# Performance work log

Measured on AMD Instinct MI355X. Metric: run time of the kernel, lower is better.

## Reference

```python
import jax, jax.numpy as jnp
import numpy as np


def _conv1x1(x, w):
    # bias-free 1x1 conv == channel-mixing GEMM: w:(out,in), x:(b,in,h,w)
    return jnp.einsum('oc,bchw->bohw', w, x)


def setup_inputs() -> dict:
    key = jax.random.key(0)
    k = jax.random.split(key, 5)
    C, IC = 512, 256  # channel, inter_channel = channel // 2
    x = jax.random.normal(k[0], (8, C, 64, 64), dtype=jnp.float32)
    s = 0.02
    return {
        'x': x,
        'w_phi': jax.random.normal(k[1], (IC, C), dtype=jnp.float32) * s,
        'w_theta': jax.random.normal(k[2], (IC, C), dtype=jnp.float32) * s,
        'w_g': jax.random.normal(k[3], (IC, C), dtype=jnp.float32) * s,
        'w_mask': jax.random.normal(k[4], (C, IC), dtype=jnp.float32) * s,
    }


def reference(x, w_phi, w_theta, w_g, w_mask):
    b, c, h, wd = x.shape
    hw = h * wd
    ic = c // 2
    # Faithful to the torch source: conv outputs have c//2 channels but are
    # viewed as (b, c, -1) -> (b, c, hw//2); tokens axis is hw//2, feat dim c.
    n = hw // 2
    phi = _conv1x1(x, w_phi).reshape(b, c, n)                      # (b, c, n)
    theta = _conv1x1(x, w_theta).reshape(b, c, n).transpose(0, 2, 1)  # (b, n, c)
    g = _conv1x1(x, w_g).reshape(b, c, n).transpose(0, 2, 1)          # (b, n, c)
    attn = jnp.einsum('bnc,bcm->bnm', theta, phi)                  # (b, n, n)
    attn = jax.nn.softmax(attn, axis=1)                            # torch Softmax(dim=1)
    out = jnp.einsum('bnm,bmc->bnc', attn, g)                      # (b, n, c)
    out = out.transpose(0, 2, 1).reshape(b, ic, h, wd)             # (b, c//2, h, w)
    return _conv1x1(out, w_mask) + x
```

## Files before the change

### kernel.cpp

```cpp
#include <hip/hip_runtime.h>

typedef unsigned short u16;
typedef __bf16 bf16x8 __attribute__((ext_vector_type(8)));
typedef unsigned short u16x8 __attribute__((ext_vector_type(8)));
typedef float f32x4 __attribute__((ext_vector_type(4)));

__device__ __forceinline__ u16 f2bf(float f) {
    unsigned u = __float_as_uint(f);
    unsigned r = u + 0x7fffu + ((u >> 16) & 1u);
    return (u16)(r >> 16);
}
__device__ __forceinline__ float bf2f(u16 v) {
    return __uint_as_float(((unsigned)v) << 16);
}

__device__ __forceinline__ void async16(const void* g, void* l) {
    __builtin_amdgcn_global_load_lds(
        (__attribute__((address_space(1))) void*)(unsigned long long)g,
        (__attribute__((address_space(3))) void*)l, 16, 0, 0);
}

__device__ __forceinline__ bf16x8 ld8(const u16* p) {
    return __builtin_bit_cast(bf16x8, *(const u16x8*)p);
}

__global__ __launch_bounds__(256) void convert_w(
        const float* __restrict__ wphi, const float* __restrict__ wtheta,
        const float* __restrict__ wg, const float* __restrict__ wm,
        u16* __restrict__ wcat, u16* __restrict__ wgb, u16* __restrict__ wmb) {
    int i = blockIdx.x * 256 + threadIdx.x;
    if (i < 131072) {
        wcat[i]          = f2bf(wphi[i]);
        wcat[131072 + i] = f2bf(wtheta[i]);
        wgb[i]           = f2bf(wg[i]);
        wmb[i]           = f2bf(wm[i]);
    }
}

__global__ __launch_bounds__(256) void transpose_convert(
        const float* __restrict__ x, u16* __restrict__ xt) {
    __shared__ float t[64][65];
    const float* xb = x + (long long)blockIdx.z * 512 * 4096;
    u16* xtb = xt + (long long)blockIdx.z * 4096 * 512;
    const int p0 = blockIdx.x * 64, c0 = blockIdx.y * 64;
    const int tp = threadIdx.x & 63, tr = threadIdx.x >> 6;
    #pragma unroll
    for (int i = 0; i < 64; i += 4)
        t[i + tr][tp] = xb[(long long)(c0 + i + tr) * 4096 + p0 + tp];
    __syncthreads();
    #pragma unroll
    for (int i = 0; i < 64; i += 4)
        xtb[(long long)(p0 + i + tr) * 512 + c0 + tp] = f2bf(t[tp][i + tr]);
}

template <int EPI>
__global__ __launch_bounds__(256) void gemm_tn(
        const u16* __restrict__ Ag, long long sA, int lda,
        const u16* __restrict__ Bg, long long sB, int ldb,
        void* __restrict__ O0, long long sO0, void* __restrict__ O1,
        const float* __restrict__ Xres, int Ksz) {
    __shared__ __align__(16) u16 As[128 * 32];
    __shared__ __align__(16) u16 Bs[128 * 32];
    const int tid = threadIdx.x;
    const int bz = blockIdx.z;
    const u16* Ab = Ag + (long long)bz * sA;
    const u16* Bb = Bg + (long long)bz * sB;
    const int tm = blockIdx.x * 128, tn = blockIdx.y * 128;
    const int lane = tid & 63, wid = tid >> 6;
    const int wr = wid >> 1, wc = wid & 1;
    const int lm = lane & 15, kg = lane >> 4;

    f32x4 zero = {0.f, 0.f, 0.f, 0.f};
    f32x4 acc[4][4];
    #pragma unroll
    for (int i = 0; i < 4; i++)
        #pragma unroll
        for (int j = 0; j < 4; j++) acc[i][j] = zero;

    const int srow = tid >> 2;
    const int scol = (tid & 3) * 8;
    const u16* a0 = Ab + (long long)(tm + srow) * lda + scol;
    const u16* a1 = Ab + (long long)(tm + 64 + srow) * lda + scol;
    const u16* b0 = Bb + (long long)(tn + srow) * ldb + scol;
    const u16* b1 = Bb + (long long)(tn + 64 + srow) * ldb + scol;
    u16* ad0 = As + tid * 8;
    u16* ad1 = As + 2048 + tid * 8;
    u16* bd0 = Bs + tid * 8;
    u16* bd1 = Bs + 2048 + tid * 8;

    for (int k0 = 0; k0 < Ksz; k0 += 32) {
        async16(a0 + k0, ad0);
        async16(a1 + k0, ad1);
        async16(b0 + k0, bd0);
        async16(b1 + k0, bd1);
        __syncthreads();
        bf16x8 af[4], bfr[4];
        #pragma unroll
        for (int i = 0; i < 4; i++) {
            af[i]  = ld8(As + (wr * 64 + i * 16 + lm) * 32 + kg * 8);
            bfr[i] = ld8(Bs + (wc * 64 + i * 16 + lm) * 32 + kg * 8);
        }
        #pragma unroll
        for (int i = 0; i < 4; i++)
            #pragma unroll
            for (int j = 0; j < 4; j++)
                acc[i][j] = __builtin_amdgcn_mfma_f32_16x16x32_bf16(af[i], bfr[j], acc[i][j], 0, 0, 0);
        __syncthreads();
    }

    if constexpr (EPI == 2) {
        #pragma unroll
        for (int j = 0; j < 4; j++) {
            const int gn = tn + wc * 64 + j * 16 + lm;
            float csum = 0.f;
            #pragma unroll
            for (int i = 0; i < 4; i++) {
                #pragma unroll
                for (int r = 0; r < 4; r++) {
                    const int gm = tm + wr * 64 + i * 16 + kg * 4 + r;
                    const float e = __expf(acc[i][j][r]);
                    ((u16*)O0)[(long long)bz * sO0 + (long long)gm * 2048 + gn] = f2bf(e);
                    csum += e;
                }
            }
            csum += __shfl_xor(csum, 16);
            csum += __shfl_xor(csum, 32);
            if (lane < 16)
                atomicAdd((float*)O1 + (long long)bz * 2048 + gn, csum);
        }
    } else {
        #pragma unroll
        for (int i = 0; i < 4; i++) {
            #pragma unroll
            for (int j = 0; j < 4; j++) {
                #pragma unroll
                for (int r = 0; r < 4; r++) {
                    const int gm = tm + wr * 64 + i * 16 + kg * 4 + r;
                    const int gn = tn + wc * 64 + j * 16 + lm;
                    const float v = acc[i][j][r];
                    if constexpr (EPI == 0) {
                        const int s = gm >> 11, mm = gm & 2047;
                        u16* dst = (u16*)(gn < 256 ? O0 : O1);
                        dst[(long long)bz * 1048576 + (long long)mm * 512 + s * 256 + (gn & 255)] = f2bf(v);
                    } else if constexpr (EPI == 1) {
                        ((u16*)O0)[(long long)bz * sO0 + (long long)gm * 4096 + gn] = f2bf(v);
                    } else if constexpr (EPI == 3) {
                        ((u16*)O0)[(long long)bz * sO0 +
                                   (long long)((((gm & 1) << 11) | gn)) * 256 + (gm >> 1)] = f2bf(v);
                    } else {
                        const long long off = (long long)bz * sO0 + (long long)gm * 4096 + gn;
                        ((float*)O0)[off] = v + Xres[off];
                    }
                }
            }
        }
    }
}

__global__ __launch_bounds__(256) void g_scale(
        u16* __restrict__ G, const float* __restrict__ S) {
    const int b = blockIdx.y;
    const long long i = ((long long)blockIdx.x * 256 + threadIdx.x) * 8;
    const int m = (int)(i & 2047);
    u16* p = G + (long long)b * 1048576 + i;
    u16x8 v = *(u16x8*)p;
    const float4 s0 = *(const float4*)(S + (long long)b * 2048 + m);
    const float4 s1 = *(const float4*)(S + (long long)b * 2048 + m + 4);
    float sv[8] = {s0.x, s0.y, s0.z, s0.w, s1.x, s1.y, s1.z, s1.w};
    u16x8 o;
    #pragma unroll
    for (int t = 0; t < 8; t++)
        o[t] = f2bf(bf2f(v[t]) / sv[t]);
    *(u16x8*)p = o;
}

extern "C" void kernel_launch(void* const* d_in, const int* in_sizes, int n_in,
                              void* d_out, int out_size, void* d_ws, size_t ws_size,
                              hipStream_t stream) {
    const float* x      = (const float*)d_in[0];
    const float* w_phi  = (const float*)d_in[1];
    const float* w_theta= (const float*)d_in[2];
    const float* w_g    = (const float*)d_in[3];
    const float* w_mask = (const float*)d_in[4];
    float* y = (float*)d_out;

    const size_t MB = 1ull << 20;
    char* ws = (char*)d_ws;

    if (ws_size >= 148 * MB) {
        u16*   xt     = (u16*)(ws);
        u16*   Z      = (u16*)(ws);
        u16*   PtL    = (u16*)(ws + 32 * MB);
        u16*   TtL    = (u16*)(ws + 48 * MB);
        u16*   G      = (u16*)(ws + 64 * MB);
        u16*   wcat   = (u16*)(ws + 80 * MB);
        u16*   wgb    = (u16*)(ws + 81 * MB);
        u16*   wmb    = (u16*)(ws + 82 * MB);
        float* colsum = (float*)(ws + 83 * MB);
        u16*   attnb  = (u16*)(ws + 84 * MB);

        convert_w<<<512, 256, 0, stream>>>(w_phi, w_theta, w_g, w_mask, wcat, wgb, wmb);
        transpose_convert<<<dim3(64, 8, 8), 256, 0, stream>>>(x, xt);
        hipMemsetAsync(colsum, 0, 8 * 2048 * sizeof(float), stream);

        gemm_tn<0><<<dim3(32, 4, 8), 256, 0, stream>>>(
            xt, 2097152, 512, wcat, 0, 512, PtL, 1048576, TtL, nullptr, 512);
        gemm_tn<1><<<dim3(2, 32, 8), 256, 0, stream>>>(
            wgb, 0, 512, xt, 2097152, 512, G, 1048576, nullptr, nullptr, 512);
        gemm_tn<2><<<dim3(16, 16, 8), 256, 0, stream>>>(
            TtL, 1048576, 512, PtL, 1048576, 512, attnb, 4194304, colsum, nullptr, 512);
        g_scale<<<dim3(512, 8), 256, 0, stream>>>(G, colsum);
        gemm_tn<3><<<dim3(4, 16, 8), 256, 0, stream>>>(
            G, 1048576, 2048, attnb, 4194304, 2048, Z, 1048576, nullptr, nullptr, 2048);
        gemm_tn<4><<<dim3(4, 32, 8), 256, 0, stream>>>(
            wmb, 0, 256, Z, 1048576, 256, y, 2097152, nullptr, x, 256);
    } else if (ws_size >= 20 * MB) {
        u16*   xt     = (u16*)(ws);
        u16*   Z      = (u16*)(ws);
        u16*   PtL    = (u16*)(ws + 4 * MB);
        u16*   TtL    = (u16*)(ws + 6 * MB);
        u16*   G      = (u16*)(ws + 8 * MB);
        u16*   attnb  = (u16*)(ws + 10 * MB);
        u16*   wcat   = (u16*)(ws + 18 * MB);
        u16*   wgb    = (u16*)(ws + 18 * MB + 512 * 1024);
        u16*   wmb    = (u16*)(ws + 18 * MB + 768 * 1024);
        float* colsum = (float*)(ws + 19 * MB);

        convert_w<<<512, 256, 0, stream>>>(w_phi, w_theta, w_g, w_mask, wcat, wgb, wmb);
        for (int b = 0; b < 8; b++) {
            const float* xb = x + (long long)b * 2097152;
            float* yb = y + (long long)b * 2097152;
            transpose_convert<<<dim3(64, 8, 1), 256, 0, stream>>>(xb, xt);
            hipMemsetAsync(colsum, 0, 2048 * sizeof(float), stream);
            gemm_tn<0><<<dim3(32, 4, 1), 256, 0, stream>>>(
                xt, 0, 512, wcat, 0, 512, PtL, 0, TtL, nullptr, 512);
            gemm_tn<1><<<dim3(2, 32, 1), 256, 0, stream>>>(
                wgb, 0, 512, xt, 0, 512, G, 0, nullptr, nullptr, 512);
            gemm_tn<2><<<dim3(16, 16, 1), 256, 0, stream>>>(
                TtL, 0, 512, PtL, 0, 512, attnb, 0, colsum, nullptr, 512);
            g_scale<<<dim3(512, 1), 256, 0, stream>>>(G, colsum);
            gemm_tn<3><<<dim3(4, 16, 1), 256, 0, stream>>>(
                G, 0, 2048, attnb, 0, 2048, Z, 0, nullptr, nullptr, 2048);
            gemm_tn<4><<<dim3(4, 32, 1), 256, 0, stream>>>(
                wmb, 0, 256, Z, 0, 256, yb, 0, nullptr, xb, 256);
        }
    }
    (void)in_sizes; (void)n_in; (void)out_size;
}
```

Baseline: 336.8 us.

## Use K=64 swizzled LDS tiles and double-buffer the long-K attention GEMM

The GEMM main loop now stages 64-wide K tiles with an XOR swizzle on the LDS column slot, which should cut bank conflicts on the fragment reads and halve the number of barriers per K. A DBUF template flag adds a double-buffered LDS pipeline that prefetches the next tile while computing the current one. Only the K=2048 attn·G GEMM uses it. LDS per block grows to 32KB single or 64KB double, which may reduce occupancy.

Result: faster. 305.9 us (-9.2%).

```diff
diff --git a/kernel.cpp b/kernel.cpp
--- a/kernel.cpp
+++ b/kernel.cpp
@@ -53,14 +53,14 @@
         xtb[(long long)(p0 + i + tr) * 512 + c0 + tp] = f2bf(t[tp][i + tr]);
 }
 
-template <int EPI>
+template <int EPI, bool DBUF>
 __global__ __launch_bounds__(256) void gemm_tn(
         const u16* __restrict__ Ag, long long sA, int lda,
         const u16* __restrict__ Bg, long long sB, int ldb,
         void* __restrict__ O0, long long sO0, void* __restrict__ O1,
         const float* __restrict__ Xres, int Ksz) {
-    __shared__ __align__(16) u16 As[128 * 32];
-    __shared__ __align__(16) u16 Bs[128 * 32];
+    __shared__ __align__(16) u16 As[DBUF ? 2 : 1][8192];
+    __shared__ __align__(16) u16 Bs[DBUF ? 2 : 1][8192];
     const int tid = threadIdx.x;
     const int bz = blockIdx.z;
     const u16* Ab = Ag + (long long)bz * sA;
@@ -77,36 +77,70 @@
         #pragma unroll
         for (int j = 0; j < 4; j++) acc[i][j] = zero;
 
-    const int srow = tid >> 2;
-    const int scol = (tid & 3) * 8;
-    const u16* a0 = Ab + (long long)(tm + srow) * lda + scol;
-    const u16* a1 = Ab + (long long)(tm + 64 + srow) * lda + scol;
-    const u16* b0 = Bb + (long long)(tn + srow) * ldb + scol;
-    const u16* b1 = Bb + (long long)(tn + 64 + srow) * ldb + scol;
-    u16* ad0 = As + tid * 8;
-    u16* ad1 = As + 2048 + tid * 8;
-    u16* bd0 = Bs + tid * 8;
-    u16* bd1 = Bs + 2048 + tid * 8;
-
-    for (int k0 = 0; k0 < Ksz; k0 += 32) {
-        async16(a0 + k0, ad0);
-        async16(a1 + k0, ad1);
-        async16(b0 + k0, bd0);
-        async16(b1 + k0, bd1);
+    const int srow = tid >> 3, sslot = tid & 7;
+    const int swk = (sslot ^ (srow & 7)) << 3;
+    const long long aoff = (long long)(tm + srow) * lda + swk;
+    const long long boff = (long long)(tn + srow) * ldb + swk;
+
+    const int s0 = (kg ^ (lm & 7)) << 3;
+    const int arow = (wr * 64 + lm) << 6;
+    const int brow = (wc * 64 + lm) << 6;
+
+#define STAGE(bi, k0) do {                                                  \
+    const u16* a_ = Ab + aoff + (k0); const u16* b_ = Bb + boff + (k0);     \
+    u16* ad = &As[bi][tid * 8];       u16* bd = &Bs[bi][tid * 8];           \
+    async16(a_,            ad);                                             \
+    async16(a_ + 32 * lda, ad + 2048);                                      \
+    async16(a_ + 64 * lda, ad + 4096);                                      \
+    async16(a_ + 96 * lda, ad + 6144);                                      \
+    async16(b_,            bd);                                             \
+    async16(b_ + 32 * ldb, bd + 2048);                                      \
+    async16(b_ + 64 * ldb, bd + 4096);                                      \
+    async16(b_ + 96 * ldb, bd + 6144);                                      \
+} while (0)
+
+#define TILE_COMPUTE(bi) do {                                               \
+    _Pragma("unroll")                                                       \
+    for (int ks = 0; ks < 2; ++ks) {                                        \
+        const int so = s0 ^ (ks << 5);                                      \
+        bf16x8 a_[4], b_[4];                                                \
+        _Pragma("unroll")                                                   \
+        for (int i = 0; i < 4; i++) {                                       \
+            a_[i] = ld8(&As[bi][arow + (i << 10) + so]);                    \
+            b_[i] = ld8(&Bs[bi][brow + (i << 10) + so]);                    \
+        }                                                                   \
+        _Pragma("unroll")                                                   \
+        for (int i = 0; i < 4; i++)                                         \
+            _Pragma("unroll")                                               \
+            for (int j = 0; j < 4; j++)                                     \
+                acc[i][j] = __builtin_amdgcn_mfma_f32_16x16x32_bf16(        \
+                    a_[i], b_[j], acc[i][j], 0, 0, 0);                      \
+    }                                                                       \
+} while (0)
+
+    const int nt = Ksz >> 6;
+    if constexpr (DBUF) {
+        STAGE(0, 0);
         __syncthreads();
-        bf16x8 af[4], bfr[4];
-        #pragma unroll
-        for (int i = 0; i < 4; i++) {
-            af[i]  = ld8(As + (wr * 64 + i * 16 + lm) * 32 + kg * 8);
-            bfr[i] = ld8(Bs + (wc * 64 + i * 16 + lm) * 32 + kg * 8);
-        }
-        #pragma unroll
-        for (int i = 0; i < 4; i++)
-            #pragma unroll
-            for (int j = 0; j < 4; j++)
-                acc[i][j] = __builtin_amdgcn_mfma_f32_16x16x32_bf16(af[i], bfr[j], acc[i][j], 0, 0, 0);
-        __syncthreads();
-    }
+        for (int t = 0; t < nt; ++t) {
+            const int cur = t & 1;
+            if (t + 1 < nt) STAGE(cur ^ 1, (t + 1) << 6);
+            TILE_COMPUTE(cur);
+            asm volatile("s_waitcnt vmcnt(0)" ::: "memory");
+            __builtin_amdgcn_sched_barrier(0);
+            __builtin_amdgcn_s_barrier();
+            __builtin_amdgcn_sched_barrier(0);
+        }
+    } else {
+        for (int t = 0; t < nt; ++t) {
+            STAGE(0, t << 6);
+            __syncthreads();
+            TILE_COMPUTE(0);
+            __syncthreads();
+        }
+    }
+#undef STAGE
+#undef TILE_COMPUTE
 
     if constexpr (EPI == 2) {
         #pragma unroll
@@ -203,16 +237,16 @@
         transpose_convert<<<dim3(64, 8, 8), 256, 0, stream>>>(x, xt);
         hipMemsetAsync(colsum, 0, 8 * 2048 * sizeof(float), stream);
 
-        gemm_tn<0><<<dim3(32, 4, 8), 256, 0, stream>>>(
+        gemm_tn<0, false><<<dim3(32, 4, 8), 256, 0, stream>>>(
             xt, 2097152, 512, wcat, 0, 512, PtL, 1048576, TtL, nullptr, 512);
-        gemm_tn<1><<<dim3(2, 32, 8), 256, 0, stream>>>(
+        gemm_tn<1, false><<<dim3(2, 32, 8), 256, 0, stream>>>(
             wgb, 0, 512, xt, 2097152, 512, G, 1048576, nullptr, nullptr, 512);
-        gemm_tn<2><<<dim3(16, 16, 8), 256, 0, stream>>>(
+        gemm_tn<2, false><<<dim3(16, 16, 8), 256, 0, stream>>>(
             TtL, 1048576, 512, PtL, 1048576, 512, attnb, 4194304, colsum, nullptr, 512);
         g_scale<<<dim3(512, 8), 256, 0, stream>>>(G, colsum);
-        gemm_tn<3><<<dim3(4, 16, 8), 256, 0, stream>>>(
+        gemm_tn<3, true><<<dim3(4, 16, 8), 256, 0, stream>>>(
             G, 1048576, 2048, attnb, 4194304, 2048, Z, 1048576, nullptr, nullptr, 2048);
-        gemm_tn<4><<<dim3(4, 32, 8), 256, 0, stream>>>(
+        gemm_tn<4, false><<<dim3(4, 32, 8), 256, 0, stream>>>(
             wmb, 0, 256, Z, 1048576, 256, y, 2097152, nullptr, x, 256);
     } else if (ws_size >= 20 * MB) {
         u16*   xt     = (u16*)(ws);
@@ -232,16 +266,16 @@
             float* yb = y + (long long)b * 2097152;
             transpose_convert<<<dim3(64, 8, 1), 256, 0, stream>>>(xb, xt);
             hipMemsetAsync(colsum, 0, 2048 * sizeof(float), stream);
-            gemm_tn<0><<<dim3(32, 4, 1), 256, 0, stream>>>(
+            gemm_tn<0, false><<<dim3(32, 4, 1), 256, 0, stream>>>(
                 xt, 0, 512, wcat, 0, 512, PtL, 0, TtL, nullptr, 512);
-            gemm_tn<1><<<dim3(2, 32, 1), 256, 0, stream>>>(
+            gemm_tn<1, false><<<dim3(2, 32, 1), 256, 0, stream>>>(
                 wgb, 0, 512, xt, 0, 512, G, 0, nullptr, nullptr, 512);
-            gemm_tn<2><<<dim3(16, 16, 1), 256, 0, stream>>>(
+            gemm_tn<2, false><<<dim3(16, 16, 1), 256, 0, stream>>>(
                 TtL, 0, 512, PtL, 0, 512, attnb, 0, colsum, nullptr, 512);
             g_scale<<<dim3(512, 1), 256, 0, stream>>>(G, colsum);
-            gemm_tn<3><<<dim3(4, 16, 1), 256, 0, stream>>>(
+            gemm_tn<3, true><<<dim3(4, 16, 1), 256, 0, stream>>>(
                 G, 0, 2048, attnb, 0, 2048, Z, 0, nullptr, nullptr, 2048);
-            gemm_tn<4><<<dim3(4, 32, 1), 256, 0, stream>>>(
+            gemm_tn<4, false><<<dim3(4, 32, 1), 256, 0, stream>>>(
                 wmb, 0, 256, Z, 0, 256, yb, 0, nullptr, xb, 256);
         }
     }
```
